# Kernel tuning notes

Measured on AMD Instinct MI355X. Metric: run time of the kernel, lower is better.

Reference implementation:

```python
import jax, jax.numpy as jnp
import numpy as np

B, L, D = 4, 2048, 1024
DK, H = 64, 16
DFF = 4 * D
MASK_FILL = -2**15 + 1  # -32767, matches masked_fill value in source


def setup_inputs() -> dict:
    key = jax.random.key(0)
    ks = jax.random.split(key, 16)
    s = lambda fan_in: 1.0 / np.sqrt(fan_in)
    inp = {
        "x": jax.random.normal(ks[0], (B, L, D), dtype=jnp.float32),
        "maskPAD": jax.random.randint(ks[1], (B, L, L), 0, 2, dtype=jnp.int32),
        # attention projections (torch Linear layout: [out, in])
        "WQ_w": jax.random.uniform(ks[2], (H * DK, D), jnp.float32, -s(D), s(D)),
        "WQ_b": jnp.zeros((H * DK,), jnp.float32),
        "WK_w": jax.random.uniform(ks[3], (H * DK, D), jnp.float32, -s(D), s(D)),
        "WK_b": jnp.zeros((H * DK,), jnp.float32),
        "WV_w": jax.random.uniform(ks[4], (H * DK, D), jnp.float32, -s(D), s(D)),
        "WV_b": jnp.zeros((H * DK,), jnp.float32),
        "WO_w": jax.random.uniform(ks[5], (D, H * DK), jnp.float32, -s(H * DK), s(H * DK)),
        "WO_b": jnp.zeros((D,), jnp.float32),
        # FFN (pre-LN inside the FFN block)
        "ln_g": jnp.ones((D,), jnp.float32),
        "ln_b": jnp.zeros((D,), jnp.float32),
        "W1_w": jax.random.uniform(ks[6], (DFF, D), jnp.float32, -s(D), s(D)),
        "W1_b": jnp.zeros((DFF,), jnp.float32),
        "W2_w": jax.random.uniform(ks[7], (D, DFF), jnp.float32, -s(DFF), s(DFF)),
        "W2_b": jnp.zeros((D,), jnp.float32),
    }
    return inp


def _layernorm(x, g, b, eps=1e-5):
    mu = jnp.mean(x, axis=-1, keepdims=True)
    var = jnp.var(x, axis=-1, keepdims=True)
    return (x - mu) * jax.lax.rsqrt(var + eps) * g + b


def reference(x, maskPAD, WQ_w, WQ_b, WK_w, WK_b, WV_w, WV_b, WO_w, WO_b,
              ln_g, ln_b, W1_w, W1_b, W2_w, W2_b):
    # --- SelfAttention_PostLN (dropout = identity at eval) ---
    q = (jnp.einsum('bld,ed->ble', x, WQ_w) + WQ_b).reshape(B, L, H, DK).transpose(0, 2, 1, 3)
    k = (jnp.einsum('bld,ed->ble', x, WK_w) + WK_b).reshape(B, L, H, DK).transpose(0, 2, 1, 3)
    v = (jnp.einsum('bld,ed->ble', x, WV_w) + WV_b).reshape(B, L, H, DK).transpose(0, 2, 1, 3)
    scores = jnp.einsum('bhqd,bhkd->bhqk', q, k) / np.sqrt(DK).astype(np.float32)
    scores = jnp.where((maskPAD == 0)[:, None, :, :], jnp.float32(MASK_FILL), scores)
    alpha = jax.nn.softmax(scores, axis=-1)
    z = jnp.einsum('bhqk,bhkd->bhqd', alpha, v)  # [B,H,L,DK]
    z = z.transpose(0, 2, 1, 3).reshape(B, L, H * DK)
    z = jnp.einsum('ble,de->bld', z, WO_w) + WO_b
    # --- FFN_PreLN ---
    r = x + z                                    # residual 1 (dropout identity)
    h = _layernorm(r, ln_g, ln_b)
    h = jax.nn.relu(jnp.einsum('bld,fd->blf', h, W1_w) + W1_b)
    h = jnp.einsum('blf,df->bld', h, W2_w) + W2_b
    return r + h
```

## Files before the change

### kernel.cpp

```cpp
#include <hip/hip_runtime.h>

#define BD      4
#define LSEQ    2048
#define DMODEL  1024
#define HHEADS  16
#define DKK     64
#define DFFN    4096
#define MROWS   (BD*LSEQ)
#define QKS     2048

typedef float  f32x4  __attribute__((ext_vector_type(4)));
typedef float  f32x16 __attribute__((ext_vector_type(16)));
typedef __bf16 bf16x8 __attribute__((ext_vector_type(8)));
typedef unsigned short u16x8 __attribute__((ext_vector_type(8)));
typedef unsigned int   u32x4 __attribute__((ext_vector_type(4)));

__device__ inline unsigned short f2bf(float x) {
    union { float f; unsigned u; } c; c.f = x;
    unsigned r = c.u + 0x7FFFu + ((c.u >> 16) & 1u);
    return (unsigned short)(r >> 16);
}

__global__ void cast_bf16_k(const float* __restrict__ in,
                            unsigned short* __restrict__ out, long n) {
    long i = ((long)blockIdx.x * blockDim.x + threadIdx.x) * 4;
    long stride = (long)gridDim.x * blockDim.x * 4;
    for (; i < n; i += stride) {
        float4 v = *(const float4*)(in + i);
        ushort4 o;
        o.x = f2bf(v.x); o.y = f2bf(v.y); o.z = f2bf(v.z); o.w = f2bf(v.w);
        *(ushort4*)(out + i) = o;
    }
}

__global__ void concat3_k(const float* __restrict__ a, const float* __restrict__ b,
                          const float* __restrict__ c, float* __restrict__ o) {
    int i = blockIdx.x * 256 + threadIdx.x;
    if (i < 1024) { o[i] = a[i]; o[1024 + i] = b[i]; o[2048 + i] = c[i]; }
}

__global__ __launch_bounds__(256) void maskbits_k(const int* __restrict__ m,
                                                  unsigned long long* __restrict__ bits) {
    const long gw = ((long)blockIdx.x * blockDim.x + threadIdx.x) >> 6;
    const int lane = threadIdx.x & 63;
    const int b   = (int)(gw >> 16);
    const int rem = (int)gw & 65535;
    const int q = rem >> 5, kt = rem & 31;
    const int v = m[((size_t)(b*LSEQ + q))*LSEQ + kt*64 + lane];
    const unsigned long long bal = __ballot(v != 0);
    if (lane == 0) bits[((size_t)(b*32 + kt))*LSEQ + q] = bal;
}

__device__ inline void gload16(const void* g, void* l) {
    __builtin_amdgcn_global_load_lds(
        (const __attribute__((address_space(1))) void*)g,
        (__attribute__((address_space(3))) void*)l, 16, 0, 0);
}

#define BAR() { __builtin_amdgcn_sched_barrier(0); __builtin_amdgcn_s_barrier(); __builtin_amdgcn_sched_barrier(0); }

#define STAGE(XSEL, XPTR, h, tau, s)                                              \
  { const unsigned short* gs0 = (XPTR) + (size_t)((h)*128 + wid*8 + srow) * K + (tau)*64 + schk*8; \
    gload16(gs0, (void*)&sm[(s)][(XSEL)][(((h)*128 + wid*8)*64)]);                 \
    gload16(gs0 + (size_t)64*K, (void*)&sm[(s)][(XSEL)][(((h)*128 + 64 + wid*8)*64)]); }

#define LDA(dst, s, mi, kk) dst = *(const bf16x8*)(&sm[(s)][0][(wr*128 + (mi)*16 + r0)*64 + ((((kk)*4 + g) ^ (r0 & 7)) << 3)]);
#define LDB(dst, s, nj, kk) dst = *(const bf16x8*)(&sm[(s)][1][(wc*64  + (nj)*16 + r0)*64 + ((((kk)*4 + g) ^ (r0 & 7)) << 3)]);

#define PHASE_MFMA(q)                                                                                   \
    __builtin_amdgcn_s_setprio(1);                                                                      \
    _Pragma("unroll")                                                                                   \
    for (int nj = 0; nj < 4; ++nj) {                                                                    \
        acc[2*(q)][nj]   = __builtin_amdgcn_mfma_f32_16x16x32_bf16(af00, bq[nj][0], acc[2*(q)][nj],   0,0,0); \
        acc[2*(q)][nj]   = __builtin_amdgcn_mfma_f32_16x16x32_bf16(af01, bq[nj][1], acc[2*(q)][nj],   0,0,0); \
        acc[2*(q)+1][nj] = __builtin_amdgcn_mfma_f32_16x16x32_bf16(af10, bq[nj][0], acc[2*(q)+1][nj], 0,0,0); \
        acc[2*(q)+1][nj] = __builtin_amdgcn_mfma_f32_16x16x32_bf16(af11, bq[nj][1], acc[2*(q)+1][nj], 0,0,0); \
    }                                                                                                   \
    __builtin_amdgcn_s_setprio(0);

#define KTILE(s, tau)                                                        \
  {                                                                          \
    const int tp1 = (tau) + 1, tp2 = (tau) + 2;                              \
    bf16x8 bq[4][2];                                                         \
    bf16x8 af00, af01, af10, af11;                                           \
    _Pragma("unroll") for (int nj = 0; nj < 4; ++nj) {                       \
        LDB(bq[nj][0], s, nj, 0); LDB(bq[nj][1], s, nj, 1); }                \
    LDA(af00, s, 0, 0); LDA(af01, s, 0, 1);                                  \
    LDA(af10, s, 1, 0); LDA(af11, s, 1, 1);                                  \
    if (tp1 < NTT) { STAGE(0, Ab, 0, tp1, (s)^1); }                          \
    BAR(); PHASE_MFMA(0); BAR();                                             \
    LDA(af00, s, 2, 0); LDA(af01, s, 2, 1);                                  \
    LDA(af10, s, 3, 0); LDA(af11, s, 3, 1);                                  \
    if (tp1 < NTT) { STAGE(0, Ab, 1, tp1, (s)^1); }                          \
    if (tp2 < NTT) { STAGE(1, Bb, 0, tp2, (s)); }                            \
    BAR(); PHASE_MFMA(1); BAR();                                             \
    LDA(af00, s, 4, 0); LDA(af01, s, 4, 1);                                  \
    LDA(af10, s, 5, 0); LDA(af11, s, 5, 1);                                  \
    if (tp2 < NTT) { STAGE(1, Bb, 1, tp2, (s)); }                            \
    BAR(); PHASE_MFMA(2); BAR();                                             \
    LDA(af00, s, 6, 0); LDA(af01, s, 6, 1);                                  \
    LDA(af10, s, 7, 0); LDA(af11, s, 7, 1);                                  \
    if (tp2 < NTT)      { asm volatile("s_waitcnt vmcnt(4)" ::: "memory"); } \
    else if (tp1 < NTT) { asm volatile("s_waitcnt vmcnt(0)" ::: "memory"); } \
    BAR(); PHASE_MFMA(3); BAR();                                             \
  }

template<int MODE, int NTT>
__global__ __launch_bounds__(512, 1) void gemm8(const unsigned short* __restrict__ A,
                                                const unsigned short* __restrict__ B,
                                                const float* __restrict__ bias,
                                                unsigned short* __restrict__ Cout,
                                                int M, int N, int K, float scaleQ)
{
    __shared__ unsigned short sm[2][2][256*64];
    const int t   = threadIdx.x;
    const int wid = t >> 6, lane = t & 63;
    const int wr  = wid >> 2, wc = wid & 3;
    const int r0  = lane & 15, g = lane >> 4;

    const int nwg = gridDim.x;
    const int bid = (blockIdx.x & 7) * (nwg >> 3) + (blockIdx.x >> 3);
    const int ntn = N >> 8;
    const int bm  = (bid / ntn) << 8, bn = (bid % ntn) << 8;

    const int srow = lane >> 3;
    const int schk = (lane & 7) ^ srow;
    const unsigned short* Ab = A + (size_t)bm * K;
    const unsigned short* Bb = B + (size_t)bn * K;

    f32x4 acc[8][4] = {};

    STAGE(1, Bb, 0, 0, 0); STAGE(1, Bb, 1, 0, 0);
    STAGE(0, Ab, 0, 0, 0); STAGE(0, Ab, 1, 0, 0);
    STAGE(1, Bb, 0, 1, 1); STAGE(1, Bb, 1, 1, 1);
    asm volatile("s_waitcnt vmcnt(4)" ::: "memory");
    BAR();

#pragma unroll 1
    for (int i2 = 0; i2 < NTT/2; ++i2) {
        const int tau = 2*i2;
        KTILE(0, tau);
        KTILE(1, tau+1);
    }

#pragma unroll
    for (int mi = 0; mi < 8; ++mi) {
        const int row0 = bm + wr*128 + mi*16 + g*4;
#pragma unroll
        for (int nj = 0; nj < 4; ++nj) {
            const int col = bn + wc*64 + nj*16 + r0;
            const float bcol = bias[col];
#pragma unroll
            for (int rr = 0; rr < 4; ++rr) {
                float c = acc[mi][nj][rr] + bcol;
                if (MODE == 1) c = fmaxf(c, 0.f);
                Cout[(size_t)(row0 + rr) * N + col] = f2bf(c);
            }
        }
    }
}

#define STAGEA2(h, tau, s)                                                        \
  { const unsigned short* gs0 = Ab + (size_t)((h)*128 + wid*8 + srow) * K + (tau)*64 + schk*8; \
    gload16(gs0, (void*)&smA[(s)][(((h)*128 + wid*8)*64)]);                        \
    gload16(gs0 + (size_t)64*K, (void*)&smA[(s)][(((h)*128 + 64 + wid*8)*64)]); }

#define STAGEB2(tau, s)                                                           \
  { const unsigned short* gs0 = Bb + (size_t)(wid*8 + srow) * K + (tau)*64 + schk*8; \
    gload16(gs0, (void*)&smB[(s)][((wid*8)*64)]);                                  \
    gload16(gs0 + (size_t)64*K, (void*)&smB[(s)][((64 + wid*8)*64)]); }

#define LDA2(dst, s, mi, kk) dst = *(const bf16x8*)(&smA[(s)][(wr*128 + (mi)*16 + r0)*64 + ((((kk)*4 + g) ^ (r0 & 7)) << 3)]);
#define LDB2(dst, s, nj, kk) dst = *(const bf16x8*)(&smB[(s)][(wc*32  + (nj)*16 + r0)*64 + ((((kk)*4 + g) ^ (r0 & 7)) << 3)]);

#define PHASE_MFMA2(q)                                                                                  \
    __builtin_amdgcn_s_setprio(1);                                                                      \
    _Pragma("unroll")                                                                                   \
    for (int nj = 0; nj < 2; ++nj) {                                                                    \
        acc[2*(q)][nj]   = __builtin_amdgcn_mfma_f32_16x16x32_bf16(af00, bq[nj][0], acc[2*(q)][nj],   0,0,0); \
        acc[2*(q)][nj]   = __builtin_amdgcn_mfma_f32_16x16x32_bf16(af01, bq[nj][1], acc[2*(q)][nj],   0,0,0); \
        acc[2*(q)+1][nj] = __builtin_amdgcn_mfma_f32_16x16x32_bf16(af10, bq[nj][0], acc[2*(q)+1][nj], 0,0,0); \
        acc[2*(q)+1][nj] = __builtin_amdgcn_mfma_f32_16x16x32_bf16(af11, bq[nj][1], acc[2*(q)+1][nj], 0,0,0); \
    }                                                                                                   \
    __builtin_amdgcn_s_setprio(0);

#define KTILE2(s, tau)                                                       \
  {                                                                          \
    const int tp1 = (tau) + 1, tp2 = (tau) + 2;                              \
    bf16x8 bq[2][2];                                                         \
    bf16x8 af00, af01, af10, af11;                                           \
    _Pragma("unroll") for (int nj = 0; nj < 2; ++nj) {                       \
        LDB2(bq[nj][0], s, nj, 0); LDB2(bq[nj][1], s, nj, 1); }              \
    LDA2(af00, s, 0, 0); LDA2(af01, s, 0, 1);                                \
    LDA2(af10, s, 1, 0); LDA2(af11, s, 1, 1);                                \
    if (tp1 < NTT) { STAGEA2(0, tp1, (s)^1); }                               \
    BAR(); PHASE_MFMA2(0); BAR();                                            \
    LDA2(af00, s, 2, 0); LDA2(af01, s, 2, 1);                                \
    LDA2(af10, s, 3, 0); LDA2(af11, s, 3, 1);                                \
    if (tp1 < NTT) { STAGEA2(1, tp1, (s)^1); }                               \
    BAR(); PHASE_MFMA2(1); BAR();                                            \
    LDA2(af00, s, 4, 0); LDA2(af01, s, 4, 1);                                \
    LDA2(af10, s, 5, 0); LDA2(af11, s, 5, 1);                                \
    if (tp2 < NTT) { STAGEB2(tp2, (s)); }                                    \
    BAR(); PHASE_MFMA2(2); BAR();                                            \
    LDA2(af00, s, 6, 0); LDA2(af01, s, 6, 1);                                \
    LDA2(af10, s, 7, 0); LDA2(af11, s, 7, 1);                                \
    if (tp2 < NTT)      { asm volatile("s_waitcnt vmcnt(2)" ::: "memory"); } \
    else if (tp1 < NTT) { asm volatile("s_waitcnt vmcnt(0)" ::: "memory"); } \
    BAR(); PHASE_MFMA2(3); BAR();                                            \
  }

template<int MODE, int NTT>
__global__ __launch_bounds__(512, 1) void gemm8n(const unsigned short* __restrict__ A,
                                                 const unsigned short* __restrict__ B,
                                                 const float* __restrict__ bias,
                                                 const float* __restrict__ resid,
                                                 void* __restrict__ Cout,
                                                 unsigned short* __restrict__ vt,
                                                 int M, int N, int K, float scaleQ)
{
    __shared__ unsigned short smA[2][256*64];
    __shared__ unsigned short smB[2][128*64];
    const int t   = threadIdx.x;
    const int wid = t >> 6, lane = t & 63;
    const int wr  = wid >> 2, wc = wid & 3;
    const int r0  = lane & 15, g = lane >> 4;

    const int nwg = gridDim.x;
    const int bid = (blockIdx.x & 7) * (nwg >> 3) + (blockIdx.x >> 3);
    const int ntn = N >> 7;
    const int bm  = (bid / ntn) << 8, bn = (bid % ntn) << 7;

    const int srow = lane >> 3;
    const int schk = (lane & 7) ^ srow;
    const unsigned short* Ab = A + (size_t)bm * K;
    const unsigned short* Bb = B + (size_t)bn * K;

    f32x4 acc[8][2] = {};

    STAGEB2(0, 0);
    STAGEA2(0, 0, 0); STAGEA2(1, 0, 0);
    STAGEB2(1, 1);
    asm volatile("s_waitcnt vmcnt(2)" ::: "memory");
    BAR();

#pragma unroll 1
    for (int i2 = 0; i2 < NTT/2; ++i2) {
        const int tau = 2*i2;
        KTILE2(0, tau);
        KTILE2(1, tau+1);
    }

#pragma unroll
    for (int mi = 0; mi < 8; ++mi) {
        const int row0 = bm + wr*128 + mi*16 + g*4;
#pragma unroll
        for (int nj = 0; nj < 2; ++nj) {
            const int col = bn + wc*32 + nj*16 + r0;
            const float bcol = bias[col];
#pragma unroll
            for (int rr = 0; rr < 4; ++rr) {
                const int row = row0 + rr;
                if (MODE == 2) {
                    float c = acc[mi][nj][rr] + bcol;
                    ((float*)Cout)[(size_t)row * N + col] = c + resid[(size_t)row * N + col];
                }
            }
            if (MODE == 3) {
                if (col < 2048) {
                    const float sc = (col < 1024) ? scaleQ : 1.0f;
#pragma unroll
                    for (int rr = 0; rr < 4; ++rr)
                        ((unsigned short*)Cout)[(size_t)(row0 + rr) * QKS + col] =
                            f2bf((acc[mi][nj][rr] + bcol) * sc);
                } else {
                    const int vcol = col - 2048;
                    const int b = row0 >> 11, tok = row0 & 2047;
                    ushort4 h4;
                    h4.x = f2bf(acc[mi][nj][0] + bcol);
                    h4.y = f2bf(acc[mi][nj][1] + bcol);
                    h4.z = f2bf(acc[mi][nj][2] + bcol);
                    h4.w = f2bf(acc[mi][nj][3] + bcol);
                    *(ushort4*)&vt[((size_t)(b*1024 + vcol))*LSEQ + tok] = h4;
                }
            }
        }
    }
}

template<int MODE>
__global__ __launch_bounds__(256) void gemm_nt(const unsigned short* __restrict__ A,
                                               const unsigned short* __restrict__ B,
                                               const float* __restrict__ bias,
                                               const float* __restrict__ resid,
                                               void* __restrict__ Cout,
                                               int M, int N, int K, float scale)
{
    __shared__ unsigned short As[128*32];
    __shared__ unsigned short Bs[128*32];
    const int t    = threadIdx.x;
    const int w    = t >> 6, lane = t & 63;
    const int r0   = lane & 15, g = lane >> 4;
    const int wm   = (w >> 1) * 64, wn = (w & 1) * 64;
    const int bm   = blockIdx.y * 128, bn = blockIdx.x * 128;
    const int srow = t >> 2, scol = (t & 3) * 8;

    const unsigned short* Ag = A + (size_t)(bm + srow) * K + scol;
    const unsigned short* Bg = B + (size_t)(bn + srow) * K + scol;
    unsigned short* AsW = As + w * 512;
    unsigned short* BsW = Bs + w * 512;

    f32x4 acc[4][4] = {};

    for (int kt = 0; kt < K; kt += 32) {
        gload16(Ag + kt,                AsW);
        gload16(Ag + (size_t)64*K + kt, AsW + 2048);
        gload16(Bg + kt,                BsW);
        gload16(Bg + (size_t)64*K + kt, BsW + 2048);
        __syncthreads();
        bf16x8 af[4], bfr[4];
#pragma unroll
        for (int i = 0; i < 4; ++i)
            af[i] = *(const bf16x8*)(As + (wm + i*16 + r0)*32 + g*8);
#pragma unroll
        for (int j = 0; j < 4; ++j)
            bfr[j] = *(const bf16x8*)(Bs + (wn + j*16 + r0)*32 + g*8);
#pragma unroll
        for (int i = 0; i < 4; ++i)
#pragma unroll
            for (int j = 0; j < 4; ++j)
                acc[i][j] = __builtin_amdgcn_mfma_f32_16x16x32_bf16(af[i], bfr[j], acc[i][j], 0, 0, 0);
        __syncthreads();
    }

#pragma unroll
    for (int i = 0; i < 4; ++i) {
        const int row0 = bm + wm + i*16 + g*4;
#pragma unroll
        for (int j = 0; j < 4; ++j) {
            const int col = bn + wn + j*16 + r0;
            const float bcol = bias[col];
#pragma unroll
            for (int rr = 0; rr < 4; ++rr) {
                const int row = row0 + rr;
                float c = (acc[i][j][rr] + bcol) * scale;
                if (MODE == 2) {
                    ((float*)Cout)[(size_t)row * N + col] = c + resid[(size_t)row * N + col];
                } else {
                    if (MODE == 1) c = fmaxf(c, 0.f);
                    ((unsigned short*)Cout)[(size_t)row * N + col] = f2bf(c);
                }
            }
        }
    }
}

#define MFILL   (-47272.79f)
#define DEFTHR  (11.5415603f)
__global__ __launch_bounds__(256) void attn_k(
    const unsigned short* __restrict__ QK,
    const unsigned short* __restrict__ VT,
    const unsigned long long* __restrict__ MBits,
    unsigned short* __restrict__ Z)
{
    __shared__ unsigned short Ks[2][64*64];
    __shared__ unsigned short Vs[2][64*64];
    __shared__ float Sc[4*32];

    const int t    = threadIdx.x;
    const int w    = t >> 6, lane = t & 63;
    const int q31  = lane & 31, hi = lane >> 5;

    const int bid = blockIdx.x;
    const int sw  = (bid & 7) * 128 + (bid >> 3);
    const int qt  = sw & 15, h = (sw >> 4) & 15, b = sw >> 8;
    const int qw  = qt * 128 + w * 32;

    const unsigned short* Qg = QK + ((size_t)(b*LSEQ + qw + q31))*QKS + h*DKK + hi*8;
    bf16x8 qf[4];
#pragma unroll
    for (int ds = 0; ds < 4; ++ds)
        qf[ds] = *(const bf16x8*)(Qg + ds*16);

    const int srow = w*8 + (lane>>3);
    const int schk = (lane & 7) ^ (srow & 7);
    const unsigned short* Kg = QK + ((size_t)(b*LSEQ))*QKS + 1024 + h*DKK;
    const unsigned short* Vg = VT + ((size_t)(b*1024 + h*DKK))*LSEQ;

    float m_r = MFILL, l_r = 0.f;
    f32x16 z0, z1;
#pragma unroll
    for (int r = 0; r < 16; ++r) { z0[r] = 0.f; z1[r] = 0.f; }

    gload16(Kg + (size_t)srow*QKS      + schk*8, &Ks[0][w*512]);
    gload16(Kg + (size_t)(32+srow)*QKS + schk*8, &Ks[0][w*512] + 2048);
    gload16(Vg + (size_t)srow*LSEQ      + schk*8, &Vs[0][w*512]);
    gload16(Vg + (size_t)(32+srow)*LSEQ + schk*8, &Vs[0][w*512] + 2048);
    unsigned long long mw = MBits[((size_t)(b*32 + 0))*LSEQ + (qw + q31)];

    for (int kt = 0; kt < LSEQ/64; ++kt) {
        const int cur = kt & 1;
        __syncthreads();

        const int ktn = (kt < LSEQ/64 - 1) ? kt + 1 : kt;
        const int k0n = ktn * 64;
        gload16(Kg + (size_t)(k0n + srow)*QKS      + schk*8, &Ks[cur^1][w*512]);
        gload16(Kg + (size_t)(k0n + 32 + srow)*QKS + schk*8, &Ks[cur^1][w*512] + 2048);
        gload16(Vg + (size_t)srow*LSEQ      + k0n + schk*8, &Vs[cur^1][w*512]);
        gload16(Vg + (size_t)(32+srow)*LSEQ + k0n + schk*8, &Vs[cur^1][w*512] + 2048);
        const unsigned long long mwn = MBits[((size_t)(b*32 + ktn))*LSEQ + (qw + q31)];

        const unsigned long long sh = mw >> (hi*4);
        const unsigned md0 = (unsigned)sh, md1 = (unsigned)(sh >> 32);

        f32x16 s0, s1;
#pragma unroll
        for (int r = 0; r < 16; ++r) { s0[r] = 0.f; s1[r] = 0.f; }
        __builtin_amdgcn_s_setprio(1);
#pragma unroll
        for (int ds = 0; ds < 4; ++ds) {
            const int slot = ((ds*2 + hi) ^ (q31 & 7)) << 3;
            bf16x8 kf0 = *(const bf16x8*)(&Ks[cur][ q31     *64 + slot]);
            bf16x8 kf1 = *(const bf16x8*)(&Ks[cur][(32+q31)*64 + slot]);
            s0 = __builtin_amdgcn_mfma_f32_32x32x16_bf16(kf0, qf[ds], s0, 0, 0, 0);
            s1 = __builtin_amdgcn_mfma_f32_32x32x16_bf16(kf1, qf[ds], s1, 0, 0, 0);
        }
        __builtin_amdgcn_s_setprio(0);

#pragma unroll
        for (int r = 0; r < 16; ++r) {
            const int kb = (r & 3) + 8*(r >> 2);
            if (!((md0 >> kb) & 1)) s0[r] = MFILL;
            if (!((md1 >> kb) & 1)) s1[r] = MFILL;
        }

        float tm = fmaxf(s0[0], s1[0]);
#pragma unroll
        for (int r = 1; r < 16; ++r) tm = fmaxf(tm, fmaxf(s0[r], s1[r]));
        {
            float ta = tm, tb = tm;
            asm volatile("v_permlane32_swap_b32 %0, %1" : "+v"(ta), "+v"(tb));
            tm = fmaxf(tm, hi ? ta : tb);
        }

        if (__any(tm > m_r + DEFTHR)) {
            const float nm   = fmaxf(m_r, tm);
            const float corr = exp2f(m_r - nm);
            Sc[w*32 + q31] = corr;
            l_r *= corr;
            m_r  = nm;
#pragma unroll
            for (int r = 0; r < 16; ++r) {
                const int row = (r & 3) + 8*(r >> 2) + 4*hi;
                const float cr = Sc[w*32 + row];
                z0[r] *= cr; z1[r] *= cr;
            }
        }

#pragma unroll
        for (int r = 0; r < 16; ++r) {
            s0[r] = exp2f(s0[r] - m_r);
            s1[r] = exp2f(s1[r] - m_r);
        }
        float r4[8];
#pragma unroll
        for (int r = 0; r < 8; ++r)
            r4[r] = (s0[2*r] + s0[2*r+1]) + (s1[2*r] + s1[2*r+1]);
        float rs = ((r4[0]+r4[1]) + (r4[2]+r4[3])) + ((r4[4]+r4[5]) + (r4[6]+r4[7]));
        {
            float ra = rs, rb = rs;
            asm volatile("v_permlane32_swap_b32 %0, %1" : "+v"(ra), "+v"(rb));
            rs += hi ? ra : rb;
        }
        l_r += rs;

        __builtin_amdgcn_s_setprio(1);
#pragma unroll
        for (int half = 0; half < 2; ++half) {
#pragma unroll
            for (int sub = 0; sub < 2; ++sub) {
                const int base = sub*8;
                unsigned wa, wb, wc2, wd;
                float p0 = half ? s1[base+0] : s0[base+0];
                float p1 = half ? s1[base+1] : s0[base+1];
                float p2 = half ? s1[base+2] : s0[base+2];
                float p3 = half ? s1[base+3] : s0[base+3];
                float p4 = half ? s1[base+4] : s0[base+4];
                float p5 = half ? s1[base+5] : s0[base+5];
                float p6 = half ? s1[base+6] : s0[base+6];
                float p7 = half ? s1[base+7] : s0[base+7];
                asm("v_cvt_pk_bf16_f32 %0, %1, %2" : "=v"(wa) : "v"(p0), "v"(p1));
                asm("v_cvt_pk_bf16_f32 %0, %1, %2" : "=v"(wb) : "v"(p4), "v"(p5));
                asm("v_cvt_pk_bf16_f32 %0, %1, %2" : "=v"(wc2) : "v"(p2), "v"(p3));
                asm("v_cvt_pk_bf16_f32 %0, %1, %2" : "=v"(wd) : "v"(p6), "v"(p7));
                asm volatile("v_permlane32_swap_b32 %0, %1" : "+v"(wa), "+v"(wb));
                asm volatile("v_permlane32_swap_b32 %0, %1" : "+v"(wc2), "+v"(wd));
                u32x4 pu; pu[0] = wa; pu[1] = wc2; pu[2] = wb; pu[3] = wd;
                bf16x8 pa = __builtin_bit_cast(bf16x8, pu);
                const int ks = half*2 + sub;
                const int slot = ((ks*2 + hi) ^ (q31 & 7)) << 3;
                bf16x8 vf0 = *(const bf16x8*)(&Vs[cur][ q31     *64 + slot]);
                bf16x8 vf1 = *(const bf16x8*)(&Vs[cur][(32+q31)*64 + slot]);
                z0 = __builtin_amdgcn_mfma_f32_32x32x16_bf16(pa, vf0, z0, 0, 0, 0);
                z1 = __builtin_amdgcn_mfma_f32_32x32x16_bf16(pa, vf1, z1, 0, 0, 0);
            }
        }
        __builtin_amdgcn_s_setprio(0);

        mw = mwn;
    }

    Sc[w*32 + q31] = l_r;
    unsigned short* Zb = Z + ((size_t)(b*LSEQ + qw))*DMODEL + h*DKK + q31;
#pragma unroll
    for (int r = 0; r < 16; ++r) {
        const int row = (r & 3) + 8*(r >> 2) + 4*hi;
        const float rl = 1.0f / Sc[w*32 + row];
        Zb[(size_t)row*DMODEL]      = f2bf(z0[r] * rl);
        Zb[(size_t)row*DMODEL + 32] = f2bf(z1[r] * rl);
    }
}

__global__ __launch_bounds__(256) void ln_k(const float* __restrict__ r,
                                            const float* __restrict__ gam,
                                            const float* __restrict__ bet,
                                            unsigned short* __restrict__ out)
{
    const int row = blockIdx.x;
    const int t = threadIdx.x;
    const float* rp = r + (size_t)row * DMODEL;
    float4 v = *(const float4*)(rp + t*4);
    float s  = v.x + v.y + v.z + v.w;
    float s2 = v.x*v.x + v.y*v.y + v.z*v.z + v.w*v.w;
#pragma unroll
    for (int off = 32; off >= 1; off >>= 1) {
        s  += __shfl_xor(s,  off);
        s2 += __shfl_xor(s2, off);
    }
    __shared__ float red[8];
    const int wv = t >> 6;
    if ((t & 63) == 0) { red[wv] = s; red[4 + wv] = s2; }
    __syncthreads();
    s  = red[0] + red[1] + red[2] + red[3];
    s2 = red[4] + red[5] + red[6] + red[7];
    const float mu   = s  * (1.f/DMODEL);
    const float var  = s2 * (1.f/DMODEL) - mu*mu;
    const float rstd = rsqrtf(var + 1e-5f);
    float4 gv = *(const float4*)(gam + t*4);
    float4 bv = *(const float4*)(bet + t*4);
    ushort4 o;
    o.x = f2bf((v.x - mu)*rstd*gv.x + bv.x);
    o.y = f2bf((v.y - mu)*rstd*gv.y + bv.y);
    o.z = f2bf((v.z - mu)*rstd*gv.z + bv.z);
    o.w = f2bf((v.w - mu)*rstd*gv.w + bv.w);
    *(ushort4*)(out + (size_t)row * DMODEL + t*4) = o;
}

extern "C" void kernel_launch(void* const* d_in, const int* in_sizes, int n_in,
                              void* d_out, int out_size, void* d_ws, size_t ws_size,
                              hipStream_t stream)
{
    const float* x    = (const float*)d_in[0];
    const int*   mask = (const int*)  d_in[1];
    const float* WQ_w = (const float*)d_in[2];
    const float* WQ_b = (const float*)d_in[3];
    const float* WK_w = (const float*)d_in[4];
    const float* WK_b = (const float*)d_in[5];
    const float* WV_w = (const float*)d_in[6];
    const float* WV_b = (const float*)d_in[7];
    const float* WO_w = (const float*)d_in[8];
    const float* WO_b = (const float*)d_in[9];
    const float* ln_g = (const float*)d_in[10];
    const float* ln_b = (const float*)d_in[11];
    const float* W1_w = (const float*)d_in[12];
    const float* W1_b = (const float*)d_in[13];
    const float* W2_w = (const float*)d_in[14];
    const float* W2_b = (const float*)d_in[15];
    float* out = (float*)d_out;

    char* w = (char*)d_ws;
    const size_t MB = 1024*1024;
    unsigned short* qk   = (unsigned short*)(w + 0*MB);
    unsigned short* vtb  = (unsigned short*)(w + 32*MB);
    unsigned short* shr  = (unsigned short*)(w + 64*MB);
    float*          rb   = (float*)         (w + 80*MB);
    unsigned short* wqkv = (unsigned short*)(w + 112*MB);
    unsigned short* wob  = (unsigned short*)(w + 118*MB);
    unsigned short* w1b  = (unsigned short*)(w + 120*MB);
    unsigned short* w2b  = (unsigned short*)(w + 128*MB);
    unsigned long long* mbits = (unsigned long long*)(w + 136*MB);
    float* bqkv = (float*)rb;
    unsigned short* xb   = shr;
    unsigned short* Zb   = shr;
    unsigned short* hln  = shr;
    unsigned short* hmid = (unsigned short*)(w + 0*MB);

    cast_bf16_k<<<2048, 256, 0, stream>>>(x,    xb,   (long)MROWS*DMODEL);
    cast_bf16_k<<<512,  256, 0, stream>>>(WQ_w, wqkv,               (long)DMODEL*DMODEL);
    cast_bf16_k<<<512,  256, 0, stream>>>(WK_w, wqkv + 1024*1024,   (long)DMODEL*DMODEL);
    cast_bf16_k<<<512,  256, 0, stream>>>(WV_w, wqkv + 2*1024*1024, (long)DMODEL*DMODEL);
    cast_bf16_k<<<512,  256, 0, stream>>>(WO_w, wob,  (long)DMODEL*DMODEL);
    cast_bf16_k<<<2048, 256, 0, stream>>>(W1_w, w1b,  (long)DFFN*DMODEL);
    cast_bf16_k<<<2048, 256, 0, stream>>>(W2_w, w2b,  (long)DMODEL*DFFN);
    maskbits_k<<<65536, 256, 0, stream>>>(mask, mbits);
    concat3_k<<<4, 256, 0, stream>>>(WQ_b, WK_b, WV_b, bqkv);

    gemm8n<3, 16><<<dim3(768), dim3(512), 0, stream>>>(xb, wqkv, bqkv, nullptr, qk, vtb,
                                                       MROWS, 3072, DMODEL, 0.18033688f);
    attn_k<<<dim3(1024), dim3(256), 0, stream>>>(qk, vtb, mbits, Zb);
    gemm_nt<2><<<dim3(8, 64), dim3(256), 0, stream>>>(Zb, wob, WO_b, x, rb, MROWS, DMODEL, DMODEL, 1.0f);
    ln_k<<<MROWS, 256, 0, stream>>>(rb, ln_g, ln_b, hln);
    gemm8<1, 16><<<dim3(512), dim3(512), 0, stream>>>(hln, w1b, W1_b, hmid,
                                                      MROWS, DFFN, DMODEL, 1.0f);
    gemm8n<2, 64><<<dim3(256), dim3(512), 0, stream>>>(hmid, w2b, W2_b, rb, out, nullptr,
                                                       MROWS, DMODEL, DFFN, 1.0f);
}
```

Before: 485.2 us.

## Route output projection through gemm8n, merge MFMA phases, apply mask post-exp

The output-projection GEMM moves from the simple single-buffered gemm_nt kernel to the pipelined gemm8n kernel, and gemm_nt is deleted. The gemm8n K-tile loop now loads eight A fragments per phase and runs two MFMA phases instead of four. This halves the barrier pairs per tile at the cost of more live registers. In attention, masked scores are no longer overwritten before the row max; they are zeroed after exp2 instead. That removes a select pass, but the running max now includes masked logits, and a fully masked row would give zeros instead of a uniform distribution.

```diff
diff --git a/kernel.cpp b/kernel.cpp
--- a/kernel.cpp
+++ b/kernel.cpp
@@ -173,14 +173,14 @@
 #define LDA2(dst, s, mi, kk) dst = *(const bf16x8*)(&smA[(s)][(wr*128 + (mi)*16 + r0)*64 + ((((kk)*4 + g) ^ (r0 & 7)) << 3)]);
 #define LDB2(dst, s, nj, kk) dst = *(const bf16x8*)(&smB[(s)][(wc*32  + (nj)*16 + r0)*64 + ((((kk)*4 + g) ^ (r0 & 7)) << 3)]);
 
-#define PHASE_MFMA2(q)                                                                                  \
+#define PHASE_MFMA2X(q0)                                                                                \
     __builtin_amdgcn_s_setprio(1);                                                                      \
     _Pragma("unroll")                                                                                   \
-    for (int nj = 0; nj < 2; ++nj) {                                                                    \
-        acc[2*(q)][nj]   = __builtin_amdgcn_mfma_f32_16x16x32_bf16(af00, bq[nj][0], acc[2*(q)][nj],   0,0,0); \
-        acc[2*(q)][nj]   = __builtin_amdgcn_mfma_f32_16x16x32_bf16(af01, bq[nj][1], acc[2*(q)][nj],   0,0,0); \
-        acc[2*(q)+1][nj] = __builtin_amdgcn_mfma_f32_16x16x32_bf16(af10, bq[nj][0], acc[2*(q)+1][nj], 0,0,0); \
-        acc[2*(q)+1][nj] = __builtin_amdgcn_mfma_f32_16x16x32_bf16(af11, bq[nj][1], acc[2*(q)+1][nj], 0,0,0); \
+    for (int mm = 0; mm < 4; ++mm) {                                                                    \
+        acc[(q0)+mm][0] = __builtin_amdgcn_mfma_f32_16x16x32_bf16(aa[2*mm],   bq[0][0], acc[(q0)+mm][0], 0,0,0); \
+        acc[(q0)+mm][0] = __builtin_amdgcn_mfma_f32_16x16x32_bf16(aa[2*mm+1], bq[0][1], acc[(q0)+mm][0], 0,0,0); \
+        acc[(q0)+mm][1] = __builtin_amdgcn_mfma_f32_16x16x32_bf16(aa[2*mm],   bq[1][0], acc[(q0)+mm][1], 0,0,0); \
+        acc[(q0)+mm][1] = __builtin_amdgcn_mfma_f32_16x16x32_bf16(aa[2*mm+1], bq[1][1], acc[(q0)+mm][1], 0,0,0); \
     }                                                                                                   \
     __builtin_amdgcn_s_setprio(0);
 
@@ -188,26 +188,26 @@
   {                                                                          \
     const int tp1 = (tau) + 1, tp2 = (tau) + 2;                              \
     bf16x8 bq[2][2];                                                         \
-    bf16x8 af00, af01, af10, af11;                                           \
-    _Pragma("unroll") for (int nj = 0; nj < 2; ++nj) {                       \
-        LDB2(bq[nj][0], s, nj, 0); LDB2(bq[nj][1], s, nj, 1); }              \
-    LDA2(af00, s, 0, 0); LDA2(af01, s, 0, 1);                                \
-    LDA2(af10, s, 1, 0); LDA2(af11, s, 1, 1);                                \
+    bf16x8 aa[8];                                                            \
+                              \
+    LDB2(bq[0][0], s, 0, 0); LDB2(bq[0][1], s, 0, 1);                        \
+    LDB2(bq[1][0], s, 1, 0); LDB2(bq[1][1], s, 1, 1);                        \
+    LDA2(aa[0], s, 0, 0); LDA2(aa[1], s, 0, 1);                              \
+    LDA2(aa[2], s, 1, 0); LDA2(aa[3], s, 1, 1);                              \
+    LDA2(aa[4], s, 2, 0); LDA2(aa[5], s, 2, 1);                              \
+    LDA2(aa[6], s, 3, 0); LDA2(aa[7], s, 3, 1);                              \
     if (tp1 < NTT) { STAGEA2(0, tp1, (s)^1); }                               \
-    BAR(); PHASE_MFMA2(0); BAR();                                            \
-    LDA2(af00, s, 2, 0); LDA2(af01, s, 2, 1);                                \
-    LDA2(af10, s, 3, 0); LDA2(af11, s, 3, 1);                                \
+    BAR(); PHASE_MFMA2X(0); BAR();                                           \
+             \
+    LDA2(aa[0], s, 4, 0); LDA2(aa[1], s, 4, 1);                              \
+    LDA2(aa[2], s, 5, 0); LDA2(aa[3], s, 5, 1);                              \
+    LDA2(aa[4], s, 6, 0); LDA2(aa[5], s, 6, 1);                              \
+    LDA2(aa[6], s, 7, 0); LDA2(aa[7], s, 7, 1);                              \
     if (tp1 < NTT) { STAGEA2(1, tp1, (s)^1); }                               \
-    BAR(); PHASE_MFMA2(1); BAR();                                            \
-    LDA2(af00, s, 4, 0); LDA2(af01, s, 4, 1);                                \
-    LDA2(af10, s, 5, 0); LDA2(af11, s, 5, 1);                                \
     if (tp2 < NTT) { STAGEB2(tp2, (s)); }                                    \
-    BAR(); PHASE_MFMA2(2); BAR();                                            \
-    LDA2(af00, s, 6, 0); LDA2(af01, s, 6, 1);                                \
-    LDA2(af10, s, 7, 0); LDA2(af11, s, 7, 1);                                \
     if (tp2 < NTT)      { asm volatile("s_waitcnt vmcnt(2)" ::: "memory"); } \
     else if (tp1 < NTT) { asm volatile("s_waitcnt vmcnt(0)" ::: "memory"); } \
-    BAR(); PHASE_MFMA2(3); BAR();                                            \
+    BAR(); PHASE_MFMA2X(4); BAR();                                           \
   }
 
 template<int MODE, int NTT>
@@ -288,73 +288,6 @@
     }
 }
 
-template<int MODE>
-__global__ __launch_bounds__(256) void gemm_nt(const unsigned short* __restrict__ A,
-                                               const unsigned short* __restrict__ B,
-                                               const float* __restrict__ bias,
-                                               const float* __restrict__ resid,
-                                               void* __restrict__ Cout,
-                                               int M, int N, int K, float scale)
-{
-    __shared__ unsigned short As[128*32];
-    __shared__ unsigned short Bs[128*32];
-    const int t    = threadIdx.x;
-    const int w    = t >> 6, lane = t & 63;
-    const int r0   = lane & 15, g = lane >> 4;
-    const int wm   = (w >> 1) * 64, wn = (w & 1) * 64;
-    const int bm   = blockIdx.y * 128, bn = blockIdx.x * 128;
-    const int srow = t >> 2, scol = (t & 3) * 8;
-
-    const unsigned short* Ag = A + (size_t)(bm + srow) * K + scol;
-    const unsigned short* Bg = B + (size_t)(bn + srow) * K + scol;
-    unsigned short* AsW = As + w * 512;
-    unsigned short* BsW = Bs + w * 512;
-
-    f32x4 acc[4][4] = {};
-
-    for (int kt = 0; kt < K; kt += 32) {
-        gload16(Ag + kt,                AsW);
-        gload16(Ag + (size_t)64*K + kt, AsW + 2048);
-        gload16(Bg + kt,                BsW);
-        gload16(Bg + (size_t)64*K + kt, BsW + 2048);
-        __syncthreads();
-        bf16x8 af[4], bfr[4];
-#pragma unroll
-        for (int i = 0; i < 4; ++i)
-            af[i] = *(const bf16x8*)(As + (wm + i*16 + r0)*32 + g*8);
-#pragma unroll
-        for (int j = 0; j < 4; ++j)
-            bfr[j] = *(const bf16x8*)(Bs + (wn + j*16 + r0)*32 + g*8);
-#pragma unroll
-        for (int i = 0; i < 4; ++i)
-#pragma unroll
-            for (int j = 0; j < 4; ++j)
-                acc[i][j] = __builtin_amdgcn_mfma_f32_16x16x32_bf16(af[i], bfr[j], acc[i][j], 0, 0, 0);
-        __syncthreads();
-    }
-
-#pragma unroll
-    for (int i = 0; i < 4; ++i) {
-        const int row0 = bm + wm + i*16 + g*4;
-#pragma unroll
-        for (int j = 0; j < 4; ++j) {
-            const int col = bn + wn + j*16 + r0;
-            const float bcol = bias[col];
-#pragma unroll
-            for (int rr = 0; rr < 4; ++rr) {
-                const int row = row0 + rr;
-                float c = (acc[i][j][rr] + bcol) * scale;
-                if (MODE == 2) {
-                    ((float*)Cout)[(size_t)row * N + col] = c + resid[(size_t)row * N + col];
-                } else {
-                    if (MODE == 1) c = fmaxf(c, 0.f);
-                    ((unsigned short*)Cout)[(size_t)row * N + col] = f2bf(c);
-                }
-            }
-        }
-    }
-}
-
 #define MFILL   (-47272.79f)
 #define DEFTHR  (11.5415603f)
 __global__ __launch_bounds__(256) void attn_k(
@@ -427,13 +360,6 @@
         }
         __builtin_amdgcn_s_setprio(0);
 
-#pragma unroll
-        for (int r = 0; r < 16; ++r) {
-            const int kb = (r & 3) + 8*(r >> 2);
-            if (!((md0 >> kb) & 1)) s0[r] = MFILL;
-            if (!((md1 >> kb) & 1)) s1[r] = MFILL;
-        }
-
         float tm = fmaxf(s0[0], s1[0]);
 #pragma unroll
         for (int r = 1; r < 16; ++r) tm = fmaxf(tm, fmaxf(s0[r], s1[r]));
@@ -459,8 +385,11 @@
 
 #pragma unroll
         for (int r = 0; r < 16; ++r) {
+            const int kb = (r & 3) + 8*(r >> 2);
             s0[r] = exp2f(s0[r] - m_r);
             s1[r] = exp2f(s1[r] - m_r);
+            if (!((md0 >> kb) & 1)) s0[r] = 0.f;
+            if (!((md1 >> kb) & 1)) s1[r] = 0.f;
         }
         float r4[8];
 #pragma unroll
@@ -608,7 +537,8 @@
     gemm8n<3, 16><<<dim3(768), dim3(512), 0, stream>>>(xb, wqkv, bqkv, nullptr, qk, vtb,
                                                        MROWS, 3072, DMODEL, 0.18033688f);
     attn_k<<<dim3(1024), dim3(256), 0, stream>>>(qk, vtb, mbits, Zb);
-    gemm_nt<2><<<dim3(8, 64), dim3(256), 0, stream>>>(Zb, wob, WO_b, x, rb, MROWS, DMODEL, DMODEL, 1.0f);
+    gemm8n<2, 16><<<dim3(256), dim3(512), 0, stream>>>(Zb, wob, WO_b, x, rb, nullptr,
+                                                       MROWS, DMODEL, DMODEL, 1.0f);
     ln_k<<<MROWS, 256, 0, stream>>>(rb, ln_g, ln_b, hln);
     gemm8<1, 16><<<dim3(512), dim3(512), 0, stream>>>(hln, w1b, W1_b, hmid,
                                                       MROWS, DFFN, DMODEL, 1.0f);
```

Result: no change. 490.0 us (+1.0%).
